# Optimization experiments

Measured on AMD Instinct MI355X. Metric: run time of the kernel, lower is better.

Reference implementation:

```python
import jax, jax.numpy as jnp
import numpy as np

DIM = 1024; DEPTH = 6; HEADS = 16; DH = 64; NF = 16; VOCAB = 20000; B = 4; N = 1024
INNER = HEADS * DH
FF_INNER = int(DIM * 4 * 2 / 3)  # GEGLU inner dim = 2730


def _ln(x, g):
    # torch F.layer_norm with beta=0 buffer, eps=1e-5
    m = x.mean(-1, keepdims=True)
    v = ((x - m) ** 2).mean(-1, keepdims=True)
    return (x - m) / jnp.sqrt(v + 1e-5) * g


def _attn(x, ctx, mask, ln_g, Wq, Wkv, Wo):
    # faithful: LayerNorm applied to x (queries); context, if given, used raw for k/v
    xn = _ln(x, ln_g)
    kv_x = xn if ctx is None else ctx
    b, i, _ = x.shape
    j = kv_x.shape[1]
    q = (xn @ Wq).reshape(b, i, HEADS, DH) * (DH ** -0.5)
    k, v = jnp.split(kv_x @ Wkv, 2, axis=-1)
    k = k.reshape(b, j, HEADS, DH)
    v = v.reshape(b, j, HEADS, DH)
    sim = jnp.einsum('bihd,bjhd->bhij', q, k)
    sim = jnp.where(mask, sim, -jnp.finfo(sim.dtype).max)
    attn = jax.nn.softmax(sim, axis=-1)
    out = jnp.einsum('bhij,bjhd->bihd', attn, v).reshape(b, i, INNER)
    return out @ Wo


def _closs(a, b, ls):
    # CLIP-style ContrastiveLossWithTemperature
    an = a / jnp.linalg.norm(a, axis=-1, keepdims=True)
    bn = b / jnp.linalg.norm(b, axis=-1, keepdims=True)
    logits = jnp.exp(ls) * (an @ bn.T)
    lab = jnp.arange(a.shape[0])
    la = -jax.nn.log_softmax(logits, axis=-1)[lab, lab].mean()
    lb = -jax.nn.log_softmax(logits.T, axis=-1)[lab, lab].mean()
    return (la + lb) * 0.5


def setup_inputs() -> dict:
    key = jax.random.key(0)
    ks = jax.random.split(key, 16)
    rn = lambda k, s: jax.random.normal(k, s, jnp.float32) * 0.02
    return {
        'spliced_data': jax.random.normal(ks[0], (B, N), jnp.float32),
        'spliced_index': jax.random.randint(ks[1], (B, N), 0, VOCAB),
        'emb': rn(ks[2], (VOCAB, DIM)),
        'fusion_tokens': jax.random.normal(ks[3], (NF, DIM), jnp.float32),
        'return_tokens': jax.random.normal(ks[4], (2, DIM), jnp.float32),
        'ln1_g': jnp.ones((DEPTH, DIM), jnp.float32),
        'Wq': rn(ks[5], (DEPTH, DIM, INNER)),
        'Wkv': rn(ks[6], (DEPTH, DIM, 2 * INNER)),
        'Wo': rn(ks[7], (DEPTH, INNER, DIM)),
        'ln2_g': jnp.ones((DEPTH, DIM), jnp.float32),
        'Wff1': rn(ks[8], (DEPTH, DIM, 2 * FF_INNER)),
        'Wff2': rn(ks[9], (DEPTH, FF_INNER, DIM)),
        'norm_g': jnp.ones((DIM,), jnp.float32),
        'pool_ln_g': jnp.ones((DIM,), jnp.float32),
        'pWq': rn(ks[10], (DIM, INNER)),
        'pWkv': rn(ks[11], (DIM, 2 * INNER)),
        'pWo': rn(ks[12], (INNER, DIM)),
        'logit_scale_c': jnp.float32(np.log(1.0 / 0.07)),
        'logit_scale_f': jnp.float32(np.log(1.0 / 0.07)),
    }


def reference(spliced_data, spliced_index, emb, fusion_tokens, return_tokens,
              ln1_g, Wq, Wkv, Wo, ln2_g, Wff1, Wff2, norm_g,
              pool_ln_g, pWq, pWkv, pWo, logit_scale_c, logit_scale_f):
    b = spliced_data.shape[0]
    # BioZorroEncoder: value-weighted embedding lookup
    spliced_tokens = emb[spliced_index] * spliced_data[..., None]  # [b, N, DIM]
    tokens = jnp.concatenate(
        [spliced_tokens, jnp.broadcast_to(fusion_tokens, (b, NF, DIM))], axis=1)
    tt = jnp.concatenate([jnp.zeros((N,), jnp.int32), jnp.ones((NF,), jnp.int32)])
    # spliced attends spliced; fusion attends everything
    zmask = (tt[:, None] == tt[None, :]) | (tt[:, None] == 1)

    def body(t, p):
        l1, wq, wkv, wo, l2, w1, w2 = p
        t = _attn(t, None, zmask, l1, wq, wkv, wo) + t
        h = _ln(t, l2) @ w1
        xh, gate = jnp.split(h, 2, axis=-1)
        t = (jax.nn.gelu(gate, approximate=False) * xh) @ w2 + t
        return t, None

    tokens, _ = jax.lax.scan(body, tokens, (ln1_g, Wq, Wkv, Wo, ln2_g, Wff1, Wff2))
    tokens = _ln(tokens, norm_g)

    rtt = jnp.array([0, 1], jnp.int32)
    pm0 = rtt[:, None] == tt[None, :]
    # faithful to source operator precedence: (pm0 | rtt) == GLOBAL(2) -> all False
    pm = (pm0.astype(jnp.int32) | rtt[:, None]) == 2

    ret = jnp.broadcast_to(return_tokens, (b, 2, DIM))
    pooled = _attn(ret, tokens, pm, pool_ln_g, pWq, pWkv, pWo) + ret

    spliced = pooled[:, 0]
    fusion = pooled[:, 1]
    loss = _closs(spliced, spliced, logit_scale_c) + _closs(spliced, fusion, logit_scale_f)
    return loss
```

## Files before the change

### kernel.cpp

```cpp
#include <hip/hip_runtime.h>

typedef unsigned short u16;
typedef unsigned long long u64;
typedef __attribute__((ext_vector_type(8))) short short8;
typedef __attribute__((ext_vector_type(4))) float f32x4;

__device__ __forceinline__ u16 f2b(float f) {
  union { float f; unsigned u; } x; x.f = f;
  unsigned r = x.u + 0x7fffu + ((x.u >> 16) & 1u);
  return (u16)(r >> 16);
}
__device__ __forceinline__ float b2f(u16 h) {
  union { unsigned u; float f; } x; x.u = ((unsigned)h) << 16;
  return x.f;
}
__device__ __forceinline__ void gld16(const void* g, void* l) {
  __builtin_amdgcn_global_load_lds(
      (__attribute__((address_space(1))) const void*)g,
      (__attribute__((address_space(3))) void*)l, 16, 0, 0);
}

__global__ __launch_bounds__(256) void embed_k(
    const float* __restrict__ data, const int* __restrict__ idx,
    const float* __restrict__ emb, const float* __restrict__ fus,
    float* __restrict__ t) {
  int row = blockIdx.x;
  int b = row / 1040, n = row % 1040;
  int tid = threadIdx.x;
  const float4* src;
  float sc = 1.f;
  if (n < 1024) {
    int e = idx[b * 1024 + n];
    sc = data[b * 1024 + n];
    src = (const float4*)(emb + (long)e * 1024);
  } else {
    src = (const float4*)(fus + (long)(n - 1024) * 1024);
  }
  float4 v = src[tid];
  v.x *= sc; v.y *= sc; v.z *= sc; v.w *= sc;
  ((float4*)(t + (long)row * 1024))[tid] = v;
}

__global__ __launch_bounds__(256) void wtrans5_k(
    const float* __restrict__ sWq, const float* __restrict__ sWkv,
    const float* __restrict__ sWo, const float* __restrict__ sW1,
    const float* __restrict__ sW2,
    u16* __restrict__ dQkvT, u16* __restrict__ dWoT,
    u16* __restrict__ dF1T, u16* __restrict__ dF2T) {
  int id = blockIdx.x;
  const float* src; u16* dst; int K, N, Kpad, nx; float sc = 1.f;
  if (id < 1024)       { src = sWq;  dst = dQkvT;             K = 1024; N = 1024; Kpad = 1024; nx = 32; sc = 0.125f; }
  else if (id < 3072)  { id -= 1024; src = sWkv; dst = dQkvT + 1024 * 1024; K = 1024; N = 2048; Kpad = 1024; nx = 64; }
  else if (id < 4096)  { id -= 3072; src = sWo;  dst = dWoT;  K = 1024; N = 1024; Kpad = 1024; nx = 32; }
  else if (id < 9600)  { id -= 4096; src = sW1;  dst = dF1T;  K = 1024; N = 5460; Kpad = 1024; nx = 172; }
  else                 { id -= 9600; src = sW2;  dst = dF2T;  K = 2730; N = 1024; Kpad = 2752; nx = 32; }
  int n0 = (id % nx) * 32, k0 = (id / nx) * 32;
  __shared__ float tile[32][33];
  int x = threadIdx.x & 31, y = threadIdx.x >> 5;
#pragma unroll
  for (int i = 0; i < 4; i++) {
    int k = k0 + y + i * 8, n = n0 + x;
    tile[y + i * 8][x] = (k < K && n < N) ? src[(long)k * N + n] * sc : 0.f;
  }
  __syncthreads();
#pragma unroll
  for (int i = 0; i < 4; i++) {
    int n = n0 + y + i * 8, k = k0 + x;
    dst[(long)n * Kpad + k] = f2b(tile[x][y + i * 8]);
  }
}

__global__ __launch_bounds__(256) void ln_k(
    const float* __restrict__ t, const float* __restrict__ g,
    u16* __restrict__ xn) {
  int row = blockIdx.x, tid = threadIdx.x;
  int wave = tid >> 6, lane = tid & 63;
  float4 v = ((const float4*)(t + (long)row * 1024))[tid];
  float s = v.x + v.y + v.z + v.w;
#pragma unroll
  for (int o = 32; o > 0; o >>= 1) s += __shfl_xor(s, o, 64);
  __shared__ float r1[4], r2[4];
  if (lane == 0) r1[wave] = s;
  __syncthreads();
  float mean = (r1[0] + r1[1] + r1[2] + r1[3]) * (1.f / 1024.f);
  float dx = v.x - mean, dy = v.y - mean, dz = v.z - mean, dw = v.w - mean;
  float q = dx * dx + dy * dy + dz * dz + dw * dw;
#pragma unroll
  for (int o = 32; o > 0; o >>= 1) q += __shfl_xor(q, o, 64);
  if (lane == 0) r2[wave] = q;
  __syncthreads();
  float var = (r2[0] + r2[1] + r2[2] + r2[3]) * (1.f / 1024.f);
  float inv = rsqrtf(var + 1e-5f);
  float4 gv = ((const float4*)g)[tid];
  u64 pack = (u64)f2b(dx * inv * gv.x)
           | ((u64)f2b(dy * inv * gv.y) << 16)
           | ((u64)f2b(dz * inv * gv.z) << 32)
           | ((u64)f2b(dw * inv * gv.w) << 48);
  *(u64*)(xn + (long)row * 1024 + tid * 4) = pack;
}

__global__ __launch_bounds__(256) void lnred_k(
    float* __restrict__ t, const float* __restrict__ p0, const float* __restrict__ p1,
    const float* __restrict__ g, u16* __restrict__ xn) {
  int row = blockIdx.x, tid = threadIdx.x;
  int wave = tid >> 6, lane = tid & 63;
  long base = (long)row * 1024;
  float4 v = ((const float4*)(t + base))[tid];
  float4 a = ((const float4*)(p0 + base))[tid];
  float4 bq = ((const float4*)(p1 + base))[tid];
  v.x += a.x + bq.x; v.y += a.y + bq.y; v.z += a.z + bq.z; v.w += a.w + bq.w;
  ((float4*)(t + base))[tid] = v;
  float s = v.x + v.y + v.z + v.w;
#pragma unroll
  for (int o = 32; o > 0; o >>= 1) s += __shfl_xor(s, o, 64);
  __shared__ float r1[4], r2[4];
  if (lane == 0) r1[wave] = s;
  __syncthreads();
  float mean = (r1[0] + r1[1] + r1[2] + r1[3]) * (1.f / 1024.f);
  float dx = v.x - mean, dy = v.y - mean, dz = v.z - mean, dw = v.w - mean;
  float q = dx * dx + dy * dy + dz * dz + dw * dw;
#pragma unroll
  for (int o = 32; o > 0; o >>= 1) q += __shfl_xor(q, o, 64);
  if (lane == 0) r2[wave] = q;
  __syncthreads();
  float var = (r2[0] + r2[1] + r2[2] + r2[3]) * (1.f / 1024.f);
  float inv = rsqrtf(var + 1e-5f);
  float4 gv = ((const float4*)g)[tid];
  u64 pack = (u64)f2b(dx * inv * gv.x)
           | ((u64)f2b(dy * inv * gv.y) << 16)
           | ((u64)f2b(dz * inv * gv.z) << 32)
           | ((u64)f2b(dw * inv * gv.w) << 48);
  *(u64*)(xn + base + tid * 4) = pack;
}

__global__ __launch_bounds__(256) void redrow_k(
    float* __restrict__ t, const float* __restrict__ p0, const float* __restrict__ p1,
    float* __restrict__ rowm, float* __restrict__ rinv) {
  int row = blockIdx.x, tid = threadIdx.x;
  int wave = tid >> 6, lane = tid & 63;
  long base = (long)row * 1024;
  float4 v = ((const float4*)(t + base))[tid];
  float4 a = ((const float4*)(p0 + base))[tid];
  float4 bq = ((const float4*)(p1 + base))[tid];
  v.x += a.x + bq.x; v.y += a.y + bq.y; v.z += a.z + bq.z; v.w += a.w + bq.w;
  ((float4*)(t + base))[tid] = v;
  float s = v.x + v.y + v.z + v.w;
#pragma unroll
  for (int o = 32; o > 0; o >>= 1) s += __shfl_xor(s, o, 64);
  __shared__ float r1[4], r2[4];
  if (lane == 0) r1[wave] = s;
  __syncthreads();
  float mean = (r1[0] + r1[1] + r1[2] + r1[3]) * (1.f / 1024.f);
  float dx = v.x - mean, dy = v.y - mean, dz = v.z - mean, dw = v.w - mean;
  float q = dx * dx + dy * dy + dz * dz + dw * dw;
#pragma unroll
  for (int o = 32; o > 0; o >>= 1) q += __shfl_xor(q, o, 64);
  if (lane == 0) r2[wave] = q;
  __syncthreads();
  if (tid == 0) {
    float var = (r2[0] + r2[1] + r2[2] + r2[3]) * (1.f / 1024.f);
    rowm[row] = mean;
    rinv[row] = rsqrtf(var + 1e-5f);
  }
}

__global__ __launch_bounds__(256) void gemm_bt(
    const u16* __restrict__ A, int lda,
    const u16* __restrict__ Bt, int ldb,
    void* __restrict__ C, int ldc,
    int K, int mode, int gx, int ns, long pstride, u16* __restrict__ vt) {
  __shared__ u16 As[3][128 * 32];
  __shared__ u16 Bs[3][128 * 32];
  int tid = threadIdx.x;
  int wave = tid >> 6, lane = tid & 63;
  int col = lane & 15, grp = lane >> 4;
  int nwg = gridDim.x;
  int id = blockIdx.x;
  int q = nwg >> 3, r = nwg & 7;
  int xcd = id & 7, off = id >> 3;
  int wgid = (xcd < r ? xcd * (q + 1) : r * (q + 1) + (xcd - r) * q) + off;
  int tiles = nwg / ns;
  int ksp = wgid / tiles;
  int rem = wgid % tiles;
  int bm = rem % gx, bn = rem / gx;
  int nst = K >> 5;
  int k0 = ((nst * ksp) / ns) << 5;
  int k1 = ((nst * (ksp + 1)) / ns) << 5;
  int sr = wave * 16 + (lane >> 2);
  int sk = ((lane & 3) ^ ((lane >> 3) & 3)) * 8;
  const u16* aSrc = A + ((long)bm * 128 + sr) * lda + sk;
  const u16* bSrc = Bt + ((long)bn * 128 + sr) * ldb + sk;
  int wm = (wave >> 1) * 64, wn = (wave & 1) * 64;
  f32x4 acc[4][4] = {};

#define GSTAGE(buf, kt) do { \
    _Pragma("unroll") \
    for (int qq = 0; qq < 2; qq++) { \
      gld16(aSrc + (kt) + (long)qq * 64 * lda, &As[buf][wave * 512 + qq * 2048]); \
      gld16(bSrc + (kt) + (long)qq * 64 * ldb, &Bs[buf][wave * 512 + qq * 2048]); \
    } } while (0)

  GSTAGE(0, k0);
  if (k0 + 32 < k1) GSTAGE(1, k0 + 32);
  int cur = 0;
  int slot = (grp ^ ((col >> 1) & 3)) * 8;
  for (int kt = k0; kt < k1; kt += 32) {
    if (kt + 64 < k1) {
      int nb = cur + 2; if (nb >= 3) nb -= 3;
      GSTAGE(nb, kt + 64);
      asm volatile("s_waitcnt vmcnt(8)" ::: "memory");
    } else if (kt + 32 < k1) {
      asm volatile("s_waitcnt vmcnt(4)" ::: "memory");
    } else {
      asm volatile("s_waitcnt vmcnt(0)" ::: "memory");
    }
    __builtin_amdgcn_s_barrier();
    __builtin_amdgcn_sched_barrier(0);
    short8 af[4], bfv[4];
#pragma unroll
    for (int m = 0; m < 4; m++)
      af[m] = *(const short8*)&As[cur][(wm + m * 16 + col) * 32 + slot];
#pragma unroll
    for (int n = 0; n < 4; n++)
      bfv[n] = *(const short8*)&Bs[cur][(wn + n * 16 + col) * 32 + slot];
    __builtin_amdgcn_s_setprio(1);
#pragma unroll
    for (int m = 0; m < 4; m++)
#pragma unroll
      for (int n = 0; n < 4; n++)
        acc[m][n] = __builtin_amdgcn_mfma_f32_16x16x32_bf16(af[m], bfv[n], acc[m][n], 0, 0, 0);
    __builtin_amdgcn_s_setprio(0);
    __builtin_amdgcn_s_barrier();
    __builtin_amdgcn_sched_barrier(0);
    cur = (cur == 2) ? 0 : cur + 1;
  }
#undef GSTAGE
  long r0 = (long)bm * 128 + wm + grp * 4;
  int c0 = bn * 128 + wn + col;
  if (mode != 1) {
    u16* Cb = (u16*)C;
#pragma unroll
    for (int m = 0; m < 4; m++)
#pragma unroll
      for (int n = 0; n < 4; n++)
#pragma unroll
        for (int rr = 0; rr < 4; rr++)
          Cb[(r0 + m * 16 + rr) * ldc + c0 + n * 16] = f2b(acc[m][n][rr]);
    if (mode == 2 && bn >= 16) {
#pragma unroll
      for (int m = 0; m < 4; m++) {
        long row = r0 + m * 16;
        if (row < 4160) {
          int bidx = (int)(row / 1040);
          int j = (int)(row - (long)bidx * 1040);
#pragma unroll
          for (int n = 0; n < 4; n++) {
            int d = c0 + n * 16 - 2048;
            u64 pack = (u64)f2b(acc[m][n][0])
                     | ((u64)f2b(acc[m][n][1]) << 16)
                     | ((u64)f2b(acc[m][n][2]) << 32)
                     | ((u64)f2b(acc[m][n][3]) << 48);
            *(u64*)(vt + ((long)(bidx * 16 + (d >> 6)) * 64 + (d & 63)) * 1040 + j) = pack;
          }
        }
      }
    }
  } else {
    float* Cf = (float*)C + (long)ksp * pstride;
#pragma unroll
    for (int m = 0; m < 4; m++)
#pragma unroll
      for (int n = 0; n < 4; n++)
#pragma unroll
        for (int rr = 0; rr < 4; rr++)
          Cf[(r0 + m * 16 + rr) * ldc + c0 + n * 16] = acc[m][n][rr];
  }
}

__global__ __launch_bounds__(256) void attn_k(
    const u16* __restrict__ qkv, const u16* __restrict__ vt,
    u16* __restrict__ out) {
  int bh = blockIdx.x, it = blockIdx.y;
  int b = bh >> 4, h = bh & 15;
  int tid = threadIdx.x, wave = tid >> 6, lane = tid & 63;
  int col = lane & 15, grp = lane >> 4;
  int i0 = it * 64;
  int jmax = (it == 16) ? 1040 : 1024;
  const u16* qb = qkv + (long)b * 1040 * 3072 + h * 64;
  const u16* kb = qkv + (long)b * 1040 * 3072 + 1024 + h * 64;
  const u16* vb = vt + (long)bh * 64 * 1040;
  __shared__ u16 Ks[2][64 * 64];
  __shared__ u16 Vs[2][64 * 64];
  __shared__ u16 Ps[4][16 * 64];

  int srow0 = wave * 8 + (lane >> 3);
  int gsw = ((lane & 7) ^ (srow0 & 7)) * 8;
#define ASTAGE(buf, j0s) do { \
    int jv = (j0s) + gsw; if (jv >= 1040) jv = 1032; \
    _Pragma("unroll") \
    for (int qq = 0; qq < 2; qq++) { \
      int rr = qq * 32 + srow0; \
      gld16(kb + (long)((j0s) + rr) * 3072 + gsw, &Ks[buf][qq * 2048 + wave * 512]); \
      gld16(vb + (long)rr * 1040 + jv, &Vs[buf][qq * 2048 + wave * 512]); \
    } } while (0)

  short8 aq[2];
  int qrow = i0 + wave * 16;
#pragma unroll
  for (int kf = 0; kf < 2; kf++)
    aq[kf] = *(const short8*)(qb + (long)(qrow + col) * 3072 + kf * 32 + grp * 8);

  short8 one8 = {};
  if (col == 0) {
#pragma unroll
    for (int i = 0; i < 8; i++) one8[i] = (short)0x3F80;
  }

  f32x4 oa[4] = {};
  f32x4 oa1 = {};

  ASTAGE(0, 0);
  int cur = 0;
  for (int j0 = 0; j0 < jmax; j0 += 64) {
    if (j0 + 64 < jmax) {
      ASTAGE(cur ^ 1, j0 + 64);
      asm volatile("s_waitcnt vmcnt(4)" ::: "memory");
    } else {
      asm volatile("s_waitcnt vmcnt(0)" ::: "memory");
    }
    __builtin_amdgcn_s_barrier();
    __builtin_amdgcn_sched_barrier(0);
    f32x4 s[4] = {};
#pragma unroll
    for (int kf = 0; kf < 2; kf++) {
      short8 bk[4];
#pragma unroll
      for (int n = 0; n < 4; n++) {
        int rk = n * 16 + col;
        bk[n] = *(const short8*)&Ks[cur][rk * 64 + ((kf * 32 + grp * 8) ^ ((rk & 7) << 3))];
      }
      __builtin_amdgcn_s_setprio(1);
#pragma unroll
      for (int n = 0; n < 4; n++)
        s[n] = __builtin_amdgcn_mfma_f32_16x16x32_bf16(aq[kf], bk[n], s[n], 0, 0, 0);
      __builtin_amdgcn_s_setprio(0);
    }
    if (j0 + 64 > jmax) {
      int lim = jmax - j0;
#pragma unroll
      for (int n = 0; n < 4; n++) {
        if (n * 16 + col >= lim) {
#pragma unroll
          for (int r = 0; r < 4; r++) s[n][r] = -1e30f;
        }
      }
    }
#pragma unroll
    for (int r = 0; r < 4; r++) {
      int rp = grp * 4 + r;
#pragma unroll
      for (int n = 0; n < 4; n++) {
        float p = __expf(s[n][r]);
        Ps[wave][rp * 64 + ((n * 16 + col) ^ ((rp & 7) << 3))] = f2b(p);
      }
    }
#pragma unroll
    for (int kf = 0; kf < 2; kf++) {
      short8 ap, bv[4];
      int rm = col;
      ap = *(const short8*)&Ps[wave][rm * 64 + ((kf * 32 + grp * 8) ^ ((rm & 7) << 3))];
#pragma unroll
      for (int n = 0; n < 4; n++) {
        int rv = n * 16 + col;
        bv[n] = *(const short8*)&Vs[cur][rv * 64 + ((kf * 32 + grp * 8) ^ ((rv & 7) << 3))];
      }
      __builtin_amdgcn_s_setprio(1);
#pragma unroll
      for (int n = 0; n < 4; n++)
        oa[n] = __builtin_amdgcn_mfma_f32_16x16x32_bf16(ap, bv[n], oa[n], 0, 0, 0);
      oa1 = __builtin_amdgcn_mfma_f32_16x16x32_bf16(ap, one8, oa1, 0, 0, 0);
      __builtin_amdgcn_s_setprio(0);
    }
    __builtin_amdgcn_s_barrier();
    __builtin_amdgcn_sched_barrier(0);
    cur ^= 1;
  }
#undef ASTAGE
  float lr[4];
#pragma unroll
  for (int r = 0; r < 4; r++) lr[r] = __shfl(oa1[r], lane & 48, 64);
#pragma unroll
  for (int n = 0; n < 4; n++)
#pragma unroll
    for (int r = 0; r < 4; r++) {
      int i = i0 + wave * 16 + grp * 4 + r;
      if (i < 1040)
        out[((long)b * 1040 + i) * 1024 + h * 64 + n * 16 + col] = f2b(oa[n][r] / lr[r]);
    }
}

__global__ __launch_bounds__(256) void act_k(
    const u16* __restrict__ h, u16* __restrict__ act) {
  int row = blockIdx.x;
  int c = blockIdx.y * 1024 + threadIdx.x * 4;
  if (c >= 2752) return;
  const u16* hr = h + (long)row * 5504;
  u64 pack = 0;
#pragma unroll
  for (int i = 0; i < 4; i++) {
    int cc = c + i;
    float r = 0.f;
    if (cc < 2730) {
      float xh = b2f(hr[cc]);
      float gt = b2f(hr[2730 + cc]);
      float ge = 0.5f * gt * (1.f + erff(gt * 0.70710678118f));
      r = ge * xh;
    }
    pack |= ((u64)f2b(r)) << (16 * i);
  }
  *(u64*)(act + (long)row * 2752 + c) = pack;
}

__global__ __launch_bounds__(256) void wcolsum_k(
    const float* __restrict__ t, const float* __restrict__ rowm,
    const float* __restrict__ rinv, float* __restrict__ colsum,
    float* __restrict__ msum) {
  int b = blockIdx.x, c = blockIdx.y, tid = threadIdx.x;
  float a0 = 0, a1 = 0, a2 = 0, a3 = 0, ms = 0;
  for (int r = 0; r < 20; r++) {
    long row = (long)b * 1040 + c * 20 + r;
    float iv = rinv[row];
    float4 v = ((const float4*)(t + row * 1024))[tid];
    a0 += v.x * iv; a1 += v.y * iv; a2 += v.z * iv; a3 += v.w * iv;
    if (tid == 0) ms += rowm[row] * iv;
  }
  atomicAdd(&colsum[b * 1024 + tid * 4 + 0], a0);
  atomicAdd(&colsum[b * 1024 + tid * 4 + 1], a1);
  atomicAdd(&colsum[b * 1024 + tid * 4 + 2], a2);
  atomicAdd(&colsum[b * 1024 + tid * 4 + 3], a3);
  if (tid == 0) atomicAdd(&msum[b], ms);
}

__global__ __launch_bounds__(256) void mv1_k(
    const float* __restrict__ colsum, const float* __restrict__ msum,
    const float* __restrict__ g, const float* __restrict__ pWkv,
    float* __restrict__ tmp) {
  int b = blockIdx.x, n = blockIdx.y * 256 + threadIdx.x;
  float msb = msum[b];
  float acc = 0.f;
  for (int k = 0; k < 1024; k++) {
    float mk = g[k] * (colsum[b * 1024 + k] - msb);
    acc += mk * pWkv[(long)k * 2048 + 1024 + n];
  }
  tmp[b * 1024 + n] = acc * (1.f / 1040.f);
}

__global__ __launch_bounds__(256) void mv2_k(
    const float* __restrict__ tmp, const float* __restrict__ pWo,
    const float* __restrict__ ret, float* __restrict__ spl,
    float* __restrict__ fub) {
  int b = blockIdx.x, n = blockIdx.y * 256 + threadIdx.x;
  float acc = 0.f;
  for (int k = 0; k < 1024; k++) acc += tmp[b * 1024 + k] * pWo[(long)k * 1024 + n];
  spl[b * 1024 + n] = ret[n] + acc;
  fub[b * 1024 + n] = ret[1024 + n] + acc;
}

__device__ float closs_dev(const float L[4][4]) {
  float la = 0.f, lb = 0.f;
  for (int i = 0; i < 4; i++) {
    float mx = fmaxf(fmaxf(L[i][0], L[i][1]), fmaxf(L[i][2], L[i][3]));
    float sm = expf(L[i][0] - mx) + expf(L[i][1] - mx) + expf(L[i][2] - mx) + expf(L[i][3] - mx);
    la += mx + logf(sm) - L[i][i];
  }
  for (int j = 0; j < 4; j++) {
    float mx = fmaxf(fmaxf(L[0][j], L[1][j]), fmaxf(L[2][j], L[3][j]));
    float sm = expf(L[0][j] - mx) + expf(L[1][j] - mx) + expf(L[2][j] - mx) + expf(L[3][j] - mx);
    lb += mx + logf(sm) - L[j][j];
  }
  return 0.125f * (la + lb);
}

__global__ __launch_bounds__(256) void loss_k(
    const float* __restrict__ s, const float* __restrict__ f,
    const float* __restrict__ lsc, const float* __restrict__ lsf,
    float* __restrict__ out) {
  __shared__ float dots[36];
  int tid = threadIdx.x, wave = tid >> 6, lane = tid & 63;
  for (int d = wave; d < 36; d += 4) {
    const float *a, *bb;
    if (d < 16) { a = s + (d >> 2) * 1024; bb = s + (d & 3) * 1024; }
    else if (d < 32) { int e = d - 16; a = s + (e >> 2) * 1024; bb = f + (e & 3) * 1024; }
    else { a = f + (d - 32) * 1024; bb = a; }
    float p = 0.f;
    for (int k = lane; k < 1024; k += 64) p += a[k] * bb[k];
#pragma unroll
    for (int o = 32; o > 0; o >>= 1) p += __shfl_xor(p, o, 64);
    if (lane == 0) dots[d] = p;
  }
  __syncthreads();
  if (tid == 0) {
    float nS[4], nF[4];
    for (int i = 0; i < 4; i++) { nS[i] = sqrtf(dots[i * 4 + i]); nF[i] = sqrtf(dots[32 + i]); }
    float e1 = expf(lsc[0]), e2 = expf(lsf[0]);
    float L1[4][4], L2[4][4];
    for (int i = 0; i < 4; i++)
      for (int j = 0; j < 4; j++) {
        L1[i][j] = e1 * dots[i * 4 + j] / (nS[i] * nS[j]);
        L2[i][j] = e2 * dots[16 + i * 4 + j] / (nS[i] * nF[j]);
      }
    out[0] = closs_dev(L1) + closs_dev(L2);
  }
}

extern "C" void kernel_launch(void* const* d_in, const int* in_sizes, int n_in,
                              void* d_out, int out_size, void* d_ws, size_t ws_size,
                              hipStream_t stream) {
  (void)in_sizes; (void)n_in; (void)out_size; (void)ws_size;
  const float* sdata = (const float*)d_in[0];
  const int*   sidx  = (const int*)d_in[1];
  const float* emb   = (const float*)d_in[2];
  const float* fus   = (const float*)d_in[3];
  const float* ret   = (const float*)d_in[4];
  const float* ln1g  = (const float*)d_in[5];
  const float* Wq    = (const float*)d_in[6];
  const float* Wkv   = (const float*)d_in[7];
  const float* Wo    = (const float*)d_in[8];
  const float* ln2g  = (const float*)d_in[9];
  const float* Wff1  = (const float*)d_in[10];
  const float* Wff2  = (const float*)d_in[11];
  const float* normg = (const float*)d_in[12];
  const float* pWkv  = (const float*)d_in[15];
  const float* pWo   = (const float*)d_in[16];
  const float* lsc   = (const float*)d_in[17];
  const float* lsf   = (const float*)d_in[18];

  char* ws = (char*)d_ws;
  float* t   = (float*)(ws + 0L);
  u16* xn    = (u16*)(ws + 17301504L);
  char* U    = ws + 25952256L;
  u16* qkv   = (u16*)(U);
  u16* vtb   = (u16*)(U + 26738688L);
  u16* aout  = (u16*)(U + 35270656L);
  u16* hb    = (u16*)(U);
  u16* ab    = (u16*)(U + 46497792L);
  float* par0 = (float*)(U);
  float* par1 = (float*)(U + 17301504L);
  char* WT   = ws + 95698944L;
  u16* qkvT  = (u16*)(WT);
  u16* WoT   = (u16*)(WT + 6291456L);
  u16* f1T   = (u16*)(WT + 8388608L);
  u16* f2T   = (u16*)(WT + 19660800L);
  char* FIN  = ws + 120995840L;
  float* rowm   = (float*)(FIN);
  float* rinvp  = (float*)(FIN + 16640L);
  float* colsum = (float*)(FIN + 33280L);
  float* msum   = (float*)(FIN + 49664L);
  float* tmp    = (float*)(FIN + 49728L);
  float* spl    = (float*)(FIN + 66112L);
  float* fub    = (float*)(FIN + 82496L);
  const long PSTR = 4224L * 1024;

  embed_k<<<4160, 256, 0, stream>>>(sdata, sidx, emb, fus, t);

  for (int l = 0; l < 6; l++) {
    wtrans5_k<<<12352, 256, 0, stream>>>(
        Wq + (long)l * 1024 * 1024, Wkv + (long)l * 1024 * 2048,
        Wo + (long)l * 1024 * 1024, Wff1 + (long)l * 1024 * 5460,
        Wff2 + (long)l * 2730 * 1024, qkvT, WoT, f1T, f2T);

    if (l == 0)
      ln_k<<<4160, 256, 0, stream>>>(t, ln1g, xn);
    else
      lnred_k<<<4160, 256, 0, stream>>>(t, par0, par1, ln1g + l * 1024, xn);

    gemm_bt<<<33 * 24, 256, 0, stream>>>(xn, 1024, qkvT, 1024, qkv, 3072, 1024, 2, 33, 1, 0, vtb);
    attn_k<<<dim3(64, 17), 256, 0, stream>>>(qkv, vtb, aout);
    gemm_bt<<<33 * 8 * 2, 256, 0, stream>>>(aout, 1024, WoT, 1024, par0, 1024, 1024, 1, 33, 2, PSTR, vtb);
    lnred_k<<<4160, 256, 0, stream>>>(t, par0, par1, ln2g + l * 1024, xn);
    gemm_bt<<<33 * 43, 256, 0, stream>>>(xn, 1024, f1T, 1024, hb, 5504, 1024, 0, 33, 1, 0, vtb);
    act_k<<<dim3(4160, 3), 256, 0, stream>>>(hb, ab);
    gemm_bt<<<33 * 8 * 2, 256, 0, stream>>>(ab, 2752, f2T, 2752, par0, 1024, 2752, 1, 33, 2, PSTR, vtb);
  }

  redrow_k<<<4160, 256, 0, stream>>>(t, par0, par1, rowm, rinvp);
  hipMemsetAsync(colsum, 0, 16448, stream);
  wcolsum_k<<<dim3(4, 52), 256, 0, stream>>>(t, rowm, rinvp, colsum, msum);
  mv1_k<<<dim3(4, 4), 256, 0, stream>>>(colsum, msum, normg, pWkv, tmp);
  mv2_k<<<dim3(4, 4), 256, 0, stream>>>(tmp, pWo, ret, spl, fub);
  loss_k<<<1, 256, 0, stream>>>(spl, fub, lsc, lsf, (float*)d_out);
}
```

Before: 1.993 ms.

## Widen GEMM tiles to 128x256 and use 4-way split-K partials

The bf16 GEMM tile grows from 128x128 to 128x256, so each wave computes 4x8 MFMA fragments and B staging loads double. This is meant to raise arithmetic intensity and cut A-tile reloads. The Wo and FF2 projections now use 4-way split-K, with partial buffers moved to a dedicated workspace region and the LN-reduce kernels summing four partials. In exchange the kernel uses more registers and LDS, and the grids get smaller, which risks lower occupancy and wave-quantisation losses; the weight padding and workspace offsets are adjusted to match.

```diff
diff --git a/kernel.cpp b/kernel.cpp
--- a/kernel.cpp
+++ b/kernel.cpp
@@ -52,8 +52,8 @@
   if (id < 1024)       { src = sWq;  dst = dQkvT;             K = 1024; N = 1024; Kpad = 1024; nx = 32; sc = 0.125f; }
   else if (id < 3072)  { id -= 1024; src = sWkv; dst = dQkvT + 1024 * 1024; K = 1024; N = 2048; Kpad = 1024; nx = 64; }
   else if (id < 4096)  { id -= 3072; src = sWo;  dst = dWoT;  K = 1024; N = 1024; Kpad = 1024; nx = 32; }
-  else if (id < 9600)  { id -= 4096; src = sW1;  dst = dF1T;  K = 1024; N = 5460; Kpad = 1024; nx = 172; }
-  else                 { id -= 9600; src = sW2;  dst = dF2T;  K = 2730; N = 1024; Kpad = 2752; nx = 32; }
+  else if (id < 9728)  { id -= 4096; src = sW1;  dst = dF1T;  K = 1024; N = 5460; Kpad = 1024; nx = 176; }
+  else                 { id -= 9728; src = sW2;  dst = dF2T;  K = 2730; N = 1024; Kpad = 2752; nx = 32; }
   int n0 = (id % nx) * 32, k0 = (id / nx) * 32;
   __shared__ float tile[32][33];
   int x = threadIdx.x & 31, y = threadIdx.x >> 5;
@@ -100,15 +100,17 @@
 }
 
 __global__ __launch_bounds__(256) void lnred_k(
-    float* __restrict__ t, const float* __restrict__ p0, const float* __restrict__ p1,
+    float* __restrict__ t, const float* __restrict__ par, long pstr,
     const float* __restrict__ g, u16* __restrict__ xn) {
   int row = blockIdx.x, tid = threadIdx.x;
   int wave = tid >> 6, lane = tid & 63;
   long base = (long)row * 1024;
   float4 v = ((const float4*)(t + base))[tid];
-  float4 a = ((const float4*)(p0 + base))[tid];
-  float4 bq = ((const float4*)(p1 + base))[tid];
-  v.x += a.x + bq.x; v.y += a.y + bq.y; v.z += a.z + bq.z; v.w += a.w + bq.w;
+#pragma unroll
+  for (int s4 = 0; s4 < 4; s4++) {
+    float4 a = ((const float4*)(par + s4 * pstr + base))[tid];
+    v.x += a.x; v.y += a.y; v.z += a.z; v.w += a.w;
+  }
   ((float4*)(t + base))[tid] = v;
   float s = v.x + v.y + v.z + v.w;
 #pragma unroll
@@ -134,15 +136,17 @@
 }
 
 __global__ __launch_bounds__(256) void redrow_k(
-    float* __restrict__ t, const float* __restrict__ p0, const float* __restrict__ p1,
+    float* __restrict__ t, const float* __restrict__ par, long pstr,
     float* __restrict__ rowm, float* __restrict__ rinv) {
   int row = blockIdx.x, tid = threadIdx.x;
   int wave = tid >> 6, lane = tid & 63;
   long base = (long)row * 1024;
   float4 v = ((const float4*)(t + base))[tid];
-  float4 a = ((const float4*)(p0 + base))[tid];
-  float4 bq = ((const float4*)(p1 + base))[tid];
-  v.x += a.x + bq.x; v.y += a.y + bq.y; v.z += a.z + bq.z; v.w += a.w + bq.w;
+#pragma unroll
+  for (int s4 = 0; s4 < 4; s4++) {
+    float4 a = ((const float4*)(par + s4 * pstr + base))[tid];
+    v.x += a.x; v.y += a.y; v.z += a.z; v.w += a.w;
+  }
   ((float4*)(t + base))[tid] = v;
   float s = v.x + v.y + v.z + v.w;
 #pragma unroll
@@ -164,13 +168,13 @@
   }
 }
 
-__global__ __launch_bounds__(256) void gemm_bt(
+__global__ __launch_bounds__(256, 2) void gemm_bt(
     const u16* __restrict__ A, int lda,
     const u16* __restrict__ Bt, int ldb,
     void* __restrict__ C, int ldc,
     int K, int mode, int gx, int ns, long pstride, u16* __restrict__ vt) {
   __shared__ u16 As[3][128 * 32];
-  __shared__ u16 Bs[3][128 * 32];
+  __shared__ u16 Bs[3][256 * 32];
   int tid = threadIdx.x;
   int wave = tid >> 6, lane = tid & 63;
   int col = lane & 15, grp = lane >> 4;
@@ -189,16 +193,18 @@
   int sr = wave * 16 + (lane >> 2);
   int sk = ((lane & 3) ^ ((lane >> 3) & 3)) * 8;
   const u16* aSrc = A + ((long)bm * 128 + sr) * lda + sk;
-  const u16* bSrc = Bt + ((long)bn * 128 + sr) * ldb + sk;
-  int wm = (wave >> 1) * 64, wn = (wave & 1) * 64;
-  f32x4 acc[4][4] = {};
+  const u16* bSrc = Bt + ((long)bn * 256 + sr) * ldb + sk;
+  int wm = (wave >> 1) * 64, wn2 = (wave & 1) * 128;
+  f32x4 acc[4][8] = {};
 
 #define GSTAGE(buf, kt) do { \
     _Pragma("unroll") \
-    for (int qq = 0; qq < 2; qq++) { \
+    for (int qq = 0; qq < 2; qq++) \
       gld16(aSrc + (kt) + (long)qq * 64 * lda, &As[buf][wave * 512 + qq * 2048]); \
+    _Pragma("unroll") \
+    for (int qq = 0; qq < 4; qq++) \
       gld16(bSrc + (kt) + (long)qq * 64 * ldb, &Bs[buf][wave * 512 + qq * 2048]); \
-    } } while (0)
+    } while (0)
 
   GSTAGE(0, k0);
   if (k0 + 32 < k1) GSTAGE(1, k0 + 32);
@@ -208,26 +214,26 @@
     if (kt + 64 < k1) {
       int nb = cur + 2; if (nb >= 3) nb -= 3;
       GSTAGE(nb, kt + 64);
-      asm volatile("s_waitcnt vmcnt(8)" ::: "memory");
+      asm volatile("s_waitcnt vmcnt(12)" ::: "memory");
     } else if (kt + 32 < k1) {
-      asm volatile("s_waitcnt vmcnt(4)" ::: "memory");
+      asm volatile("s_waitcnt vmcnt(6)" ::: "memory");
     } else {
       asm volatile("s_waitcnt vmcnt(0)" ::: "memory");
     }
     __builtin_amdgcn_s_barrier();
     __builtin_amdgcn_sched_barrier(0);
-    short8 af[4], bfv[4];
+    short8 af[4], bfv[8];
 #pragma unroll
     for (int m = 0; m < 4; m++)
       af[m] = *(const short8*)&As[cur][(wm + m * 16 + col) * 32 + slot];
 #pragma unroll
-    for (int n = 0; n < 4; n++)
-      bfv[n] = *(const short8*)&Bs[cur][(wn + n * 16 + col) * 32 + slot];
+    for (int n = 0; n < 8; n++)
+      bfv[n] = *(const short8*)&Bs[cur][(wn2 + n * 16 + col) * 32 + slot];
     __builtin_amdgcn_s_setprio(1);
 #pragma unroll
     for (int m = 0; m < 4; m++)
 #pragma unroll
-      for (int n = 0; n < 4; n++)
+      for (int n = 0; n < 8; n++)
         acc[m][n] = __builtin_amdgcn_mfma_f32_16x16x32_bf16(af[m], bfv[n], acc[m][n], 0, 0, 0);
     __builtin_amdgcn_s_setprio(0);
     __builtin_amdgcn_s_barrier();
@@ -236,17 +242,17 @@
   }
 #undef GSTAGE
   long r0 = (long)bm * 128 + wm + grp * 4;
-  int c0 = bn * 128 + wn + col;
+  int c0 = bn * 256 + wn2 + col;
   if (mode != 1) {
     u16* Cb = (u16*)C;
 #pragma unroll
     for (int m = 0; m < 4; m++)
 #pragma unroll
-      for (int n = 0; n < 4; n++)
+      for (int n = 0; n < 8; n++)
 #pragma unroll
         for (int rr = 0; rr < 4; rr++)
           Cb[(r0 + m * 16 + rr) * ldc + c0 + n * 16] = f2b(acc[m][n][rr]);
-    if (mode == 2 && bn >= 16) {
+    if (mode == 2 && bn >= 8) {
 #pragma unroll
       for (int m = 0; m < 4; m++) {
         long row = r0 + m * 16;
@@ -254,7 +260,7 @@
           int bidx = (int)(row / 1040);
           int j = (int)(row - (long)bidx * 1040);
 #pragma unroll
-          for (int n = 0; n < 4; n++) {
+          for (int n = 0; n < 8; n++) {
             int d = c0 + n * 16 - 2048;
             u64 pack = (u64)f2b(acc[m][n][0])
                      | ((u64)f2b(acc[m][n][1]) << 16)
@@ -270,7 +276,7 @@
 #pragma unroll
     for (int m = 0; m < 4; m++)
 #pragma unroll
-      for (int n = 0; n < 4; n++)
+      for (int n = 0; n < 8; n++)
 #pragma unroll
         for (int rr = 0; rr < 4; rr++)
           Cf[(r0 + m * 16 + rr) * ldc + c0 + n * 16] = acc[m][n][rr];
@@ -404,7 +410,7 @@
   int row = blockIdx.x;
   int c = blockIdx.y * 1024 + threadIdx.x * 4;
   if (c >= 2752) return;
-  const u16* hr = h + (long)row * 5504;
+  const u16* hr = h + (long)row * 5632;
   u64 pack = 0;
 #pragma unroll
   for (int i = 0; i < 4; i++) {
@@ -543,15 +549,13 @@
   u16* vtb   = (u16*)(U + 26738688L);
   u16* aout  = (u16*)(U + 35270656L);
   u16* hb    = (u16*)(U);
-  u16* ab    = (u16*)(U + 46497792L);
-  float* par0 = (float*)(U);
-  float* par1 = (float*)(U + 17301504L);
-  char* WT   = ws + 95698944L;
+  u16* ab    = (u16*)(U + 47579136L);
+  char* WT   = ws + 96780288L;
   u16* qkvT  = (u16*)(WT);
   u16* WoT   = (u16*)(WT + 6291456L);
   u16* f1T   = (u16*)(WT + 8388608L);
-  u16* f2T   = (u16*)(WT + 19660800L);
-  char* FIN  = ws + 120995840L;
+  u16* f2T   = (u16*)(WT + 19922944L);
+  char* FIN  = ws + 122339328L;
   float* rowm   = (float*)(FIN);
   float* rinvp  = (float*)(FIN + 16640L);
   float* colsum = (float*)(FIN + 33280L);
@@ -559,12 +563,13 @@
   float* tmp    = (float*)(FIN + 49728L);
   float* spl    = (float*)(FIN + 66112L);
   float* fub    = (float*)(FIN + 82496L);
+  float* par    = (float*)(ws + 123000000L);
   const long PSTR = 4224L * 1024;
 
   embed_k<<<4160, 256, 0, stream>>>(sdata, sidx, emb, fus, t);
 
   for (int l = 0; l < 6; l++) {
-    wtrans5_k<<<12352, 256, 0, stream>>>(
+    wtrans5_k<<<12480, 256, 0, stream>>>(
         Wq + (long)l * 1024 * 1024, Wkv + (long)l * 1024 * 2048,
         Wo + (long)l * 1024 * 1024, Wff1 + (long)l * 1024 * 5460,
         Wff2 + (long)l * 2730 * 1024, qkvT, WoT, f1T, f2T);
@@ -572,18 +577,18 @@
     if (l == 0)
       ln_k<<<4160, 256, 0, stream>>>(t, ln1g, xn);
     else
-      lnred_k<<<4160, 256, 0, stream>>>(t, par0, par1, ln1g + l * 1024, xn);
-
-    gemm_bt<<<33 * 24, 256, 0, stream>>>(xn, 1024, qkvT, 1024, qkv, 3072, 1024, 2, 33, 1, 0, vtb);
+      lnred_k<<<4160, 256, 0, stream>>>(t, par, PSTR, ln1g + l * 1024, xn);
+
+    gemm_bt<<<33 * 12, 256, 0, stream>>>(xn, 1024, qkvT, 1024, qkv, 3072, 1024, 2, 33, 1, 0, vtb);
     attn_k<<<dim3(64, 17), 256, 0, stream>>>(qkv, vtb, aout);
-    gemm_bt<<<33 * 8 * 2, 256, 0, stream>>>(aout, 1024, WoT, 1024, par0, 1024, 1024, 1, 33, 2, PSTR, vtb);
-    lnred_k<<<4160, 256, 0, stream>>>(t, par0, par1, ln2g + l * 1024, xn);
-    gemm_bt<<<33 * 43, 256, 0, stream>>>(xn, 1024, f1T, 1024, hb, 5504, 1024, 0, 33, 1, 0, vtb);
+    gemm_bt<<<33 * 4 * 4, 256, 0, stream>>>(aout, 1024, WoT, 1024, par, 1024, 1024, 1, 33, 4, PSTR, vtb);
+    lnred_k<<<4160, 256, 0, stream>>>(t, par, PSTR, ln2g + l * 1024, xn);
+    gemm_bt<<<33 * 22, 256, 0, stream>>>(xn, 1024, f1T, 1024, hb, 5632, 1024, 0, 33, 1, 0, vtb);
     act_k<<<dim3(4160, 3), 256, 0, stream>>>(hb, ab);
-    gemm_bt<<<33 * 8 * 2, 256, 0, stream>>>(ab, 2752, f2T, 2752, par0, 1024, 2752, 1, 33, 2, PSTR, vtb);
-  }
-
-  redrow_k<<<4160, 256, 0, stream>>>(t, par0, par1, rowm, rinvp);
+    gemm_bt<<<33 * 4 * 4, 256, 0, stream>>>(ab, 2752, f2T, 2752, par, 1024, 2752, 1, 33, 4, PSTR, vtb);
+  }
+
+  redrow_k<<<4160, 256, 0, stream>>>(t, par, PSTR, rowm, rinvp);
   hipMemsetAsync(colsum, 0, 16448, stream);
   wcolsum_k<<<dim3(4, 52), 256, 0, stream>>>(t, rowm, rinvp, colsum, msum);
   mv1_k<<<dim3(4, 4), 256, 0, stream>>>(colsum, msum, normg, pWkv, tmp);
```

Result: slower. 2.166 ms (+8.7%).
